# Kernel optimization log

Measured on AMD Instinct MI355X. Metric: run time of the kernel, lower is better.

Reference implementation:

```python
import jax, jax.numpy as jnp
import numpy as np

DIM = 1024
HEADS = 16
HEAD_DIM = 64
WINDOW = 64


def setup_inputs() -> dict:
    key = jax.random.key(0)
    ks = jax.random.split(key, 9)
    s = lambda fan_in: 1.0 / np.sqrt(fan_in)
    x = jax.random.normal(ks[0], (2, 2048, DIM), dtype=jnp.float32)
    # KANEXLayer: phi = Linear(dim, hidden=dim) -> SiLU -> Linear(dim, dim); g = Linear(dim, 3*H*D)
    W1 = jax.random.uniform(ks[1], (DIM, DIM), jnp.float32, -s(DIM), s(DIM))
    b1 = jax.random.uniform(ks[2], (DIM,), jnp.float32, -s(DIM), s(DIM))
    W2 = jax.random.uniform(ks[3], (DIM, DIM), jnp.float32, -s(DIM), s(DIM))
    b2 = jax.random.uniform(ks[4], (DIM,), jnp.float32, -s(DIM), s(DIM))
    Wg = jax.random.uniform(ks[5], (3 * HEADS * HEAD_DIM, DIM), jnp.float32, -s(DIM), s(DIM))
    bg = jax.random.uniform(ks[6], (3 * HEADS * HEAD_DIM,), jnp.float32, -s(DIM), s(DIM))
    Wo = jax.random.uniform(ks[7], (DIM, HEADS * HEAD_DIM), jnp.float32, -s(HEADS * HEAD_DIM), s(HEADS * HEAD_DIM))
    bo = jax.random.uniform(ks[8], (DIM,), jnp.float32, -s(HEADS * HEAD_DIM), s(HEADS * HEAD_DIM))
    return {"x": x, "W1": W1, "b1": b1, "W2": W2, "b2": b2,
            "Wg": Wg, "bg": bg, "Wo": Wo, "bo": bo}


def reference(x, W1, b1, W2, b2, Wg, bg, Wo, bo):
    b, n, _ = x.shape
    # KANEXLayer: g(phi(x))
    h = jax.nn.silu(x @ W1.T + b1) @ W2.T + b2          # [b, n, dim]
    qkv = h @ Wg.T + bg                                  # [b, n, 3*H*D]
    q, k, v = jnp.split(qkv, 3, axis=-1)
    reshape = lambda t: t.reshape(b, n, HEADS, HEAD_DIM).transpose(0, 2, 1, 3)  # [b, H, n, D]
    q, k, v = reshape(q), reshape(k), reshape(v)
    dots = jnp.einsum('bhid,bhjd->bhij', q, k) * (HEAD_DIM ** -0.5)  # [b, H, n, n]
    # mask positions j >= i + window (triu with diagonal=window_size)
    i = jnp.arange(n)[:, None]
    j = jnp.arange(n)[None, :]
    mask = j >= i + WINDOW                               # [n, n] bool
    dots = jnp.where(mask, -jnp.inf, dots)
    attn = jax.nn.softmax(dots, axis=-1)
    out = jnp.einsum('bhij,bhjd->bhid', attn, v)         # [b, H, n, D]
    out = out.transpose(0, 2, 1, 3).reshape(b, n, HEADS * HEAD_DIM)
    return out @ Wo.T + bo                               # [b, n, dim]
```

## Files before the change

kernel.cpp:

```cpp
#include <hip/hip_runtime.h>

typedef unsigned short u16;
typedef unsigned int   u32;
typedef __bf16 bf16x8 __attribute__((ext_vector_type(8)));
typedef float  f32x4  __attribute__((ext_vector_type(4)));

__device__ __forceinline__ u16 f2bf(float f) {
    return __builtin_bit_cast(u16, (__bf16)f);
}

__device__ __forceinline__ void gload16(const void* g, void* lds) {
    __builtin_amdgcn_global_load_lds(
        (const __attribute__((address_space(1))) u32*)g,
        (__attribute__((address_space(3))) u32*)lds, 16, 0, 0);
}

__device__ __forceinline__ f32x4 mfma16(bf16x8 a, bf16x8 b, f32x4 c) {
    return __builtin_amdgcn_mfma_f32_16x16x32_bf16(a, b, c, 0, 0, 0);
}

__global__ __launch_bounds__(256) void k_cvt5(const float* __restrict__ x,
                                              const float* __restrict__ W1,
                                              const float* __restrict__ W2,
                                              const float* __restrict__ Wg,
                                              const float* __restrict__ Wo,
                                              u16* __restrict__ xb, u16* __restrict__ w1b,
                                              u16* __restrict__ w2b, u16* __restrict__ wgb,
                                              u16* __restrict__ wob) {
    int i = blockIdx.x * 256 + threadIdx.x;
    const float* src; u16* dst; int off;
    if (i < 1048576)      { src = x;  dst = xb;  off = 0; }
    else if (i < 1310720) { src = W1; dst = w1b; off = 1048576; }
    else if (i < 1572864) { src = W2; dst = w2b; off = 1310720; }
    else if (i < 2359296) { src = Wg; dst = wgb; off = 1572864; }
    else                  { src = Wo; dst = wob; off = 2359296; }
    int j = i - off;
    float4 v = ((const float4*)src)[j];
    ushort4 o;
    o.x = f2bf(v.x); o.y = f2bf(v.y); o.z = f2bf(v.z); o.w = f2bf(v.w);
    ((ushort4*)dst)[j] = o;
}

template<bool SILU, bool OUT_BF16, bool VTOUT>
__global__ __launch_bounds__(512) void k_gemm(const u16* __restrict__ A,
                                              const u16* __restrict__ B,
                                              const float* __restrict__ bias,
                                              void* __restrict__ Cout,
                                              int M, int N, int K, int qcols,
                                              u16* __restrict__ vtout) {
    __shared__ __align__(16) u16 As[2][128 * 64];
    __shared__ __align__(16) u16 Bs[2][128 * 64];
    const int tid = threadIdx.x;
    const int w = tid >> 6, l = tid & 63;
    const int wm = w >> 2, wn = w & 3;
    const int lr = l & 15, lg = l >> 4;

    const int nwg = gridDim.x * gridDim.y;
    const int hw = blockIdx.x + gridDim.x * blockIdx.y;
    const int wg = (hw & 7) * (nwg >> 3) + (hw >> 3);
    const int m0 = (wg % gridDim.x) * 128, n0 = (wg / gridDim.x) * 128;

    f32x4 acc[4][2];
#pragma unroll
    for (int i = 0; i < 4; ++i)
#pragma unroll
        for (int j = 0; j < 2; ++j) acc[i][j] = (f32x4){0.f, 0.f, 0.f, 0.f};

    const int srow = l >> 3;
    const int ss = (l & 7) ^ (srow & 7);
    auto STAGE = [&](int buf, int kt) {
#pragma unroll
        for (int i = 0; i < 4; ++i) {
            const int g = w * 4 + i;
            if (g < 16)
                gload16(&A[(size_t)(m0 + g * 8 + srow) * K + kt * 64 + ss * 8],
                        &As[buf][g * 512]);
            else
                gload16(&B[(size_t)(n0 + (g - 16) * 8 + srow) * K + kt * 64 + ss * 8],
                        &Bs[buf][(g - 16) * 512]);
        }
    };

    const int nkt = K >> 6;
    STAGE(0, 0);
    __syncthreads();
    for (int kt = 0; kt < nkt; ++kt) {
        const int cur = kt & 1;
        if (kt + 1 < nkt) STAGE(cur ^ 1, kt + 1);
#pragma unroll
        for (int s = 0; s < 2; ++s) {
            bf16x8 af[4], bq[2];
#pragma unroll
            for (int f = 0; f < 4; ++f) {
                const int r = wm * 64 + f * 16 + lr;
                af[f] = *(const bf16x8*)&As[cur][r * 64 + (((s * 4 + lg) ^ (r & 7)) * 8)];
            }
#pragma unroll
            for (int n = 0; n < 2; ++n) {
                const int r = wn * 32 + n * 16 + lr;
                bq[n] = *(const bf16x8*)&Bs[cur][r * 64 + (((s * 4 + lg) ^ (r & 7)) * 8)];
            }
#pragma unroll
            for (int mf = 0; mf < 4; ++mf)
#pragma unroll
                for (int nf = 0; nf < 2; ++nf)
                    acc[mf][nf] = mfma16(af[mf], bq[nf], acc[mf][nf]);
        }
        if (kt + 1 < nkt) __syncthreads();
    }

    if (VTOUT && n0 >= 2048) {
        __syncthreads();
        u16* tl = &As[0][0];
#pragma unroll
        for (int nf = 0; nf < 2; ++nf) {
            const int cl = wn * 32 + nf * 16 + lr;
            const float bv = bias[n0 + cl];
            const int xr = (cl & 7) << 4;
#pragma unroll
            for (int mf = 0; mf < 4; ++mf) {
#pragma unroll
                for (int r = 0; r < 4; ++r) {
                    const int ml = wm * 64 + mf * 16 + lg * 4 + r;
                    tl[cl * 128 + (ml ^ xr)] = f2bf(acc[mf][nf][r] + bv);
                }
            }
        }
        __syncthreads();
        const int dl = tid >> 2;
        const int t0 = (tid & 3) * 32;
        const int dfull = (n0 - 2048) + dl;
        const int bhg = (m0 >> 11) * 16 + (dfull >> 6);
        const size_t vrow = (size_t)(bhg * 64 + (dfull & 63)) * 2048 + (m0 & 2047) + t0;
        const int xr = (dl & 7) << 4;
#pragma unroll
        for (int c = 0; c < 4; ++c) {
            bf16x8 vv = *(const bf16x8*)&tl[dl * 128 + ((t0 + c * 8) ^ xr)];
            *(bf16x8*)&vtout[vrow + c * 8] = vv;
        }
        return;
    }
#pragma unroll
    for (int nf = 0; nf < 2; ++nf) {
        const int col = n0 + wn * 32 + nf * 16 + lr;
        const float bv = bias[col];
        const float cs = (col < qcols) ? 0.18033688011112042f : 1.0f;
#pragma unroll
        for (int mf = 0; mf < 4; ++mf) {
            float vv[4];
#pragma unroll
            for (int r = 0; r < 4; ++r) {
                float v = acc[mf][nf][r] + bv;
                if (SILU) v = v / (1.0f + __expf(-v));
                vv[r] = v * cs;
            }
            const int row0 = m0 + wm * 64 + mf * 16 + lg * 4;
            if (OUT_BF16) {
#pragma unroll
                for (int r = 0; r < 4; ++r)
                    ((u16*)Cout)[(size_t)(row0 + r) * N + col] = f2bf(vv[r]);
            } else {
#pragma unroll
                for (int r = 0; r < 4; ++r)
                    ((float*)Cout)[(size_t)(row0 + r) * N + col] = vv[r];
            }
        }
    }
}

__device__ __forceinline__ void attn_leg(const u16* __restrict__ Ksb,
                                         const u16* __restrict__ Vsb,
                                         u16* __restrict__ Plw,
                                         int lr, int lg, bf16x8 q0, bf16x8 q1,
                                         f32x4 (&o)[4], float& ls,
                                         int thr, bool domask) {
    f32x4 st[4];
#pragma unroll
    for (int f = 0; f < 4; ++f) st[f] = (f32x4){0.f, 0.f, 0.f, 0.f};
    __builtin_amdgcn_s_setprio(1);
#pragma unroll
    for (int s = 0; s < 2; ++s) {
        const bf16x8 qf = s ? q1 : q0;
#pragma unroll
        for (int f = 0; f < 4; ++f) {
            const int row = f * 16 + lr;
            const int sw = ((s * 4 + lg) ^ (row & 7)) * 8;
            bf16x8 kf = *(const bf16x8*)&Ksb[row * 64 + sw];
            st[f] = mfma16(kf, qf, st[f]);
        }
    }
    __builtin_amdgcn_s_setprio(0);
    const int kbase = lg * 4;
#pragma unroll
    for (int f = 0; f < 4; ++f) {
        float pv[4];
#pragma unroll
        for (int r = 0; r < 4; ++r) {
            float sv = st[f][r];
            if (domask) sv = (f * 16 + kbase + r > thr) ? -1e30f : sv;
            pv[r] = exp2f(sv);
            ls += pv[r];
        }
        ushort4 pw;
        pw.x = f2bf(pv[0]); pw.y = f2bf(pv[1]); pw.z = f2bf(pv[2]); pw.w = f2bf(pv[3]);
        *(ushort4*)&Plw[lr * 80 + f * 16 + kbase] = pw;
    }
    __builtin_amdgcn_s_setprio(1);
#pragma unroll
    for (int s = 0; s < 2; ++s) {
        const bf16x8 pf = *(const bf16x8*)&Plw[lr * 80 + s * 32 + lg * 8];
#pragma unroll
        for (int f = 0; f < 4; ++f) {
            const int row = f * 16 + lr;
            const int sw = ((s * 4 + lg) ^ (row & 7)) * 8;
            bf16x8 vf = *(const bf16x8*)&Vsb[row * 64 + sw];
            o[f] = mfma16(pf, vf, o[f]);
        }
    }
    __builtin_amdgcn_s_setprio(0);
}

__global__ __launch_bounds__(512) void k_attn(const u16* __restrict__ qkv,
                                              const u16* __restrict__ vt,
                                              u16* __restrict__ ao) {
    __shared__ __align__(16) u16 Ks[2][64 * 64];
    __shared__ __align__(16) u16 Vs[2][64 * 64];
    __shared__ __align__(16) u16 Pl[8][16 * 80];
    const int hw = blockIdx.x + 16 * blockIdx.y;
    const int xcd = hw & 7, u = hw >> 3;
    const int um = u & 15;
    const int p = (u < 32) ? um : (15 - um);
    const int bh = xcd * 4 + (u >> 4);
    const int b = bh >> 4, h = bh & 15;
    const int tid = threadIdx.x, w = tid >> 6, l = tid & 63;
    const int lr = l & 15, lg = l >> 4;
    const int i = (w >> 2) ? (2 * p + 1) : (2 * p);
    const int nt = min(i + 2, 32);
    const int ntL = min(2 * p + 3, 32);

    const size_t qb = (size_t)(b * 2048 + i * 64 + (w & 3) * 16 + lr) * 3072 + h * 64;
    const bf16x8 q0 = *(const bf16x8*)&qkv[qb + lg * 8];
    const bf16x8 q1 = *(const bf16x8*)&qkv[qb + 32 + lg * 8];

    f32x4 o[4];
#pragma unroll
    for (int f = 0; f < 4; ++f) o[f] = (f32x4){0.f, 0.f, 0.f, 0.f};
    float ls = 0.f;
    const int ql = i * 64 + (w & 3) * 16 + lr;

    const int srow = tid >> 3;
    const int ss = (tid & 7) ^ (srow & 7);
    auto STAGE = [&](int buf, int t) {
        const int j0 = t * 64;
        gload16(&qkv[(size_t)(b * 2048 + j0 + srow) * 3072 + 1024 + h * 64 + ss * 8],
                &Ks[buf][tid * 8]);
        gload16(&vt[(size_t)(bh * 64 + srow) * 2048 + j0 + ss * 8], &Vs[buf][tid * 8]);
    };

    STAGE(0, 0);
    __syncthreads();
    for (int t = 0; t < ntL; ++t) {
        const int cur = t & 1;
        if (t + 1 < ntL) STAGE(cur ^ 1, t + 1);
        if (t < nt)
            attn_leg(Ks[cur], Vs[cur], Pl[w], lr, lg, q0, q1, o, ls,
                     ql + 63 - t * 64, t == nt - 1);
        __syncthreads();
    }

    ls += __shfl_xor(ls, 16); ls += __shfl_xor(ls, 32);
    float li[4];
#pragma unroll
    for (int r = 0; r < 4; ++r) li[r] = 1.0f / __shfl(ls, lg * 4 + r);
#pragma unroll
    for (int f = 0; f < 4; ++f) {
#pragma unroll
        for (int r = 0; r < 4; ++r) {
            const int row = b * 2048 + i * 64 + (w & 3) * 16 + lg * 4 + r;
            ao[(size_t)row * 1024 + h * 64 + f * 16 + lr] = f2bf(o[f][r] * li[r]);
        }
    }
}

extern "C" void kernel_launch(void* const* d_in, const int* in_sizes, int n_in,
                              void* d_out, int out_size, void* d_ws, size_t ws_size,
                              hipStream_t stream) {
    const float* x  = (const float*)d_in[0];
    const float* W1 = (const float*)d_in[1];
    const float* b1 = (const float*)d_in[2];
    const float* W2 = (const float*)d_in[3];
    const float* b2 = (const float*)d_in[4];
    const float* Wg = (const float*)d_in[5];
    const float* bg = (const float*)d_in[6];
    const float* Wo = (const float*)d_in[7];
    const float* bo = (const float*)d_in[8];
    float* out = (float*)d_out;

    char* ws = (char*)d_ws;
    const size_t MB = 1024 * 1024;
    u16* x_bf   = (u16*)(ws + 0);
    u16* w1_bf  = (u16*)(ws + 8  * MB);
    u16* w2_bf  = (u16*)(ws + 10 * MB);
    u16* wg_bf  = (u16*)(ws + 12 * MB);
    u16* wo_bf  = (u16*)(ws + 18 * MB);
    u16* h1_bf  = (u16*)(ws + 20 * MB);
    u16* h_bf   = (u16*)(ws + 28 * MB);
    u16* qkv_bf = (u16*)(ws + 36 * MB);
    u16* vt_bf  = (u16*)(ws + 60 * MB);
    u16* ao_bf  = (u16*)(ws + 68 * MB);

    k_cvt5<<<10240, 256, 0, stream>>>(x, W1, W2, Wg, Wo,
                                      x_bf, w1_bf, w2_bf, wg_bf, wo_bf);

    k_gemm<true,  true,  false><<<dim3(32, 8),  512, 0, stream>>>(x_bf,  w1_bf, b1, h1_bf,  4096, 1024, 1024, 0, nullptr);
    k_gemm<false, true,  false><<<dim3(32, 8),  512, 0, stream>>>(h1_bf, w2_bf, b2, h_bf,   4096, 1024, 1024, 0, nullptr);
    k_gemm<false, true,  true ><<<dim3(32, 24), 512, 0, stream>>>(h_bf,  wg_bf, bg, qkv_bf, 4096, 3072, 1024, 1024, vt_bf);

    k_attn<<<dim3(16, 32), 512, 0, stream>>>(qkv_bf, vt_bf, ao_bf);

    k_gemm<false, false, false><<<dim3(32, 8), 512, 0, stream>>>(ao_bf, wo_bf, bo, out, 4096, 1024, 1024, 0, nullptr);
}
```

Measured before the change: 161.7 us.

## Triple-buffer GEMM k-loop and balance attention query-tile pairing per block

The GEMM moves from double to triple LDS buffering and prefetches two k-tiles ahead. It replaces __syncthreads with an explicit vmcnt wait plus s_barrier, so global loads overlap compute more deeply. This raises LDS use per block to 96KB, which may reduce occupancy. The attention kernel now pairs query tile p with tile 31-p in each block rather than adjacent tiles, which evens out the number of key tiles each block processes.

```diff
diff --git a/kernel.cpp b/kernel.cpp
--- a/kernel.cpp
+++ b/kernel.cpp
@@ -48,8 +48,8 @@
                                               void* __restrict__ Cout,
                                               int M, int N, int K, int qcols,
                                               u16* __restrict__ vtout) {
-    __shared__ __align__(16) u16 As[2][128 * 64];
-    __shared__ __align__(16) u16 Bs[2][128 * 64];
+    __shared__ __align__(16) u16 As[3][128 * 64];
+    __shared__ __align__(16) u16 Bs[3][128 * 64];
     const int tid = threadIdx.x;
     const int w = tid >> 6, l = tid & 63;
     const int wm = w >> 2, wn = w & 3;
@@ -83,22 +83,26 @@
 
     const int nkt = K >> 6;
     STAGE(0, 0);
-    __syncthreads();
+    STAGE(1, 1);
+    asm volatile("s_waitcnt vmcnt(4)" ::: "memory");
+    __builtin_amdgcn_s_barrier();
+    __builtin_amdgcn_sched_barrier(0);
     for (int kt = 0; kt < nkt; ++kt) {
-        const int cur = kt & 1;
-        if (kt + 1 < nkt) STAGE(cur ^ 1, kt + 1);
+        if (kt + 2 < nkt) STAGE((kt + 2) % 3, kt + 2);
+        const u16* Ac = As[kt % 3];
+        const u16* Bc = Bs[kt % 3];
 #pragma unroll
         for (int s = 0; s < 2; ++s) {
             bf16x8 af[4], bq[2];
 #pragma unroll
             for (int f = 0; f < 4; ++f) {
                 const int r = wm * 64 + f * 16 + lr;
-                af[f] = *(const bf16x8*)&As[cur][r * 64 + (((s * 4 + lg) ^ (r & 7)) * 8)];
+                af[f] = *(const bf16x8*)&Ac[r * 64 + (((s * 4 + lg) ^ (r & 7)) * 8)];
             }
 #pragma unroll
             for (int n = 0; n < 2; ++n) {
                 const int r = wn * 32 + n * 16 + lr;
-                bq[n] = *(const bf16x8*)&Bs[cur][r * 64 + (((s * 4 + lg) ^ (r & 7)) * 8)];
+                bq[n] = *(const bf16x8*)&Bc[r * 64 + (((s * 4 + lg) ^ (r & 7)) * 8)];
             }
 #pragma unroll
             for (int mf = 0; mf < 4; ++mf)
@@ -106,7 +110,12 @@
                 for (int nf = 0; nf < 2; ++nf)
                     acc[mf][nf] = mfma16(af[mf], bq[nf], acc[mf][nf]);
         }
-        if (kt + 1 < nkt) __syncthreads();
+        if (kt + 1 < nkt) {
+            if (kt + 2 < nkt) asm volatile("s_waitcnt vmcnt(4)" ::: "memory");
+            else              asm volatile("s_waitcnt vmcnt(0)" ::: "memory");
+            __builtin_amdgcn_s_barrier();
+            __builtin_amdgcn_sched_barrier(0);
+        }
     }
 
     if (VTOUT && n0 >= 2048) {
@@ -227,16 +236,14 @@
     __shared__ __align__(16) u16 Vs[2][64 * 64];
     __shared__ __align__(16) u16 Pl[8][16 * 80];
     const int hw = blockIdx.x + 16 * blockIdx.y;
-    const int xcd = hw & 7, u = hw >> 3;
-    const int um = u & 15;
-    const int p = (u < 32) ? um : (15 - um);
-    const int bh = xcd * 4 + (u >> 4);
+    const int logical = (hw & 7) * 64 + (hw >> 3);
+    const int p = logical & 15, bh = logical >> 4;
     const int b = bh >> 4, h = bh & 15;
     const int tid = threadIdx.x, w = tid >> 6, l = tid & 63;
     const int lr = l & 15, lg = l >> 4;
-    const int i = (w >> 2) ? (2 * p + 1) : (2 * p);
+    const int i = (w >> 2) ? (31 - p) : p;
     const int nt = min(i + 2, 32);
-    const int ntL = min(2 * p + 3, 32);
+    const int ntL = min(33 - p, 32);
 
     const size_t qb = (size_t)(b * 2048 + i * 64 + (w & 3) * 16 + lr) * 3072 + h * 64;
     const bf16x8 q0 = *(const bf16x8*)&qkv[qb + lg * 8];
```

After: 161.9 us. No clear change (+0.1%).
